# Kernel optimization log

Hardware: AMD Instinct MI355X
Metric: run time of the kernel (lower is better)

The kernel has to match this reference:

```python
import jax, jax.numpy as jnp
import numpy as np

NUM_HEADS = 8
DIM = 256
NUM_Q = 1


def setup_inputs() -> dict:
    key = jax.random.key(0)
    ks = jax.random.split(key, 10)
    B, H, W, C = 4, 56, 56, DIM
    mask_h = mask_w = 7
    WinNum = mask_h * mask_w
    x = jax.random.normal(ks[0], (B, H, W, C), dtype=jnp.float32)
    clstoken = jax.random.normal(ks[1], (B, NUM_Q, C), dtype=jnp.float32)
    mask = jax.random.bernoulli(ks[2], 0.3, (B, WinNum, WinNum))
    # ensure each window attends to itself (avoid fully-masked rows)
    eye = jnp.eye(WinNum, dtype=bool)[None]
    mask = jnp.logical_or(mask, eye)
    Wqkv = jax.random.normal(ks[3], (C, 3 * C), dtype=jnp.float32) * (C ** -0.5)
    bqkv = jnp.zeros((3 * C,), dtype=jnp.float32)
    Wo = jax.random.normal(ks[4], (C, C), dtype=jnp.float32) * (C ** -0.5)
    bo = jnp.zeros((C,), dtype=jnp.float32)
    lepe_k = jax.random.normal(ks[5], (3, 3, 1, C), dtype=jnp.float32) * 0.1  # depthwise HWIO
    lepe_b = jnp.zeros((C,), dtype=jnp.float32)
    return {"x": x, "clstoken": clstoken, "mask": mask, "mask_h": mask_h,
            "mask_w": mask_w, "Wqkv": Wqkv, "bqkv": bqkv, "Wo": Wo, "bo": bo,
            "lepe_k": lepe_k, "lepe_b": lepe_b}


def _forward(x, clstoken, mask, mask_h, mask_w, Wqkv, bqkv, Wo, bo, lepe_k, lepe_b):
    B, H, W, C = x.shape
    num_q = clstoken.shape[1]
    Nh = NUM_HEADS
    Hd = C // Nh
    Win_h, Win_w = H // mask_h, W // mask_w
    WinPix = Win_h * Win_w
    WinNum = mask_h * mask_w
    L_win = H * W
    scale = C ** -0.5

    qkv = x @ Wqkv + bqkv                       # [B,H,W,3C]
    q, k, v = jnp.split(qkv, 3, axis=-1)
    qkv_cls = clstoken @ Wqkv + bqkv            # [B,Q,3C]
    q_cls, k_cls, v_cls = jnp.split(qkv_cls, 3, axis=-1)

    # depthwise lepe conv on v (NHWC)
    lepe = jax.lax.conv_general_dilated(
        v, lepe_k, window_strides=(1, 1), padding='SAME',
        dimension_numbers=('NHWC', 'HWIO', 'NHWC'), feature_group_count=C) + lepe_b

    def to_win(t):  # b (j h)(i w)(Nh Hd) -> b Nh (j i h w) Hd
        t = t.reshape(B, mask_h, Win_h, mask_w, Win_w, Nh, Hd)
        t = t.transpose(0, 5, 1, 3, 2, 4, 6)
        return t.reshape(B, Nh, L_win, Hd)

    def cls_heads(t):  # b q (Nh Hd) -> b Nh q Hd
        return t.reshape(B, num_q, Nh, Hd).transpose(0, 2, 1, 3)

    q_all = jnp.concatenate([to_win(q), cls_heads(q_cls)], axis=2)
    k_all = jnp.concatenate([to_win(k), cls_heads(k_cls)], axis=2)
    v_all = jnp.concatenate([to_win(v), cls_heads(v_cls)], axis=2)

    # token-level block mask; cls block (id WinNum) is globally visible
    blk = jnp.concatenate([jnp.arange(L_win) // WinPix,
                           jnp.full((num_q,), WinNum)])
    mask_ext = jnp.pad(mask, ((0, 0), (0, 1), (0, 1)), constant_values=True)
    tok_mask = mask_ext[:, blk[:, None], blk[None, :]]  # [B,L,L]

    scores = jnp.einsum('bnqd,bnkd->bnqk', q_all, k_all) * scale
    neg = jnp.finfo(scores.dtype).min
    scores = jnp.where(tok_mask[:, None], scores, neg)
    attn = jax.nn.softmax(scores, axis=-1)
    out = jnp.einsum('bnqk,bnkd->bnqd', attn, v_all)   # [B,Nh,L,Hd]

    cls_out = out[:, :, -num_q:, :]
    x_out = out[:, :, :-num_q, :]
    # b Nh (j i h w) Hd -> b (j h)(i w)(Nh Hd)
    x_out = x_out.reshape(B, Nh, mask_h, mask_w, Win_h, Win_w, Hd)
    x_out = x_out.transpose(0, 2, 4, 3, 5, 1, 6).reshape(B, H, W, C)
    cls_out = cls_out.transpose(0, 2, 1, 3).reshape(B, num_q, C)

    x_out = (x_out + lepe) @ Wo + bo
    cls_out = cls_out @ Wo + bo
    return x_out, cls_out


def reference(x, clstoken, mask, mask_h, mask_w, Wqkv, bqkv, Wo, bo, lepe_k, lepe_b):
    return _forward(x, clstoken, mask, mask_h, mask_w, Wqkv, bqkv, Wo, bo, lepe_k, lepe_b)
```

## Files before the change

kernel.cpp:

```cpp
#include <hip/hip_runtime.h>
#include <math.h>

#define B_      4
#define NH      8
#define HD      32
#define WINNUM  49
#define LWIN    3136
#define NTOK    3137
#define NPIX    12544
#define MROWS   12548
#define SCALE_L2E 0.09016844005556021f
#define SM_BIAS   4.0f

typedef _Float16 half_t;
using half8 = __attribute__((ext_vector_type(8))) half_t;
using half4 = __attribute__((ext_vector_type(4))) half_t;
using f32x4 = __attribute__((ext_vector_type(4))) float;

__device__ __forceinline__ unsigned pack2(float a, float b) {
    auto h = __builtin_amdgcn_cvt_pkrtz(a, b);
    return __builtin_bit_cast(unsigned, h);
}

__global__ __launch_bounds__(256)
void prep(const float* __restrict__ x, const float* __restrict__ cls,
          const float* __restrict__ Wqkv, const float* __restrict__ Wo,
          half_t* __restrict__ xh, half_t* __restrict__ Wqkvt, half_t* __restrict__ Wot)
{
    const int idx = blockIdx.x * 256 + threadIdx.x;
    const int stride = gridDim.x * 256;
    for (int i = idx; i < MROWS * 256; i += stride) {
        int row = i >> 8, c = i & 255;
        float v = (row < NPIX) ? x[i] : cls[(row - NPIX) * 256 + c];
        xh[i] = (half_t)v;
    }
    for (int i = idx; i < 768 * 256; i += stride) {
        int n = i >> 8, k = i & 255;
        Wqkvt[i] = (half_t)Wqkv[k * 768 + n];
    }
    for (int i = idx; i < 256 * 256; i += stride) {
        int n = i >> 8, k = i & 255;
        Wot[i] = (half_t)Wo[k * 256 + n];
    }
}

__global__ __launch_bounds__(256)
void qkv_gemm(const half_t* __restrict__ xh, const half_t* __restrict__ Bt,
              const float* __restrict__ bqkv,
              half_t* __restrict__ qh, half_t* __restrict__ kh,
              half_t* __restrict__ khcls, half_t* __restrict__ vh,
              half_t* __restrict__ vplain)
{
    __shared__ __align__(16) short As[2][128 * 40];
    __shared__ __align__(16) short Bs[2][128 * 40];
    const int m0 = blockIdx.y * 128, n0 = blockIdx.x * 128;
    const int tid = threadIdx.x;
    const int lane = tid & 63, wv = tid >> 6;
    const int wm = wv >> 1, wn = wv & 1;
    const int qi = lane & 15, g = lane >> 4;
    f32x4 acc[4][4] = {};

    int4 ra[2], rb[2];
    auto issue = [&](int k0) {
#pragma unroll
        for (int i = 0; i < 2; ++i) {
            int ch = tid + 256 * i;
            int row = ch >> 2, kc = (ch & 3) * 8;
            int m = m0 + row;
            ra[i] = (m < MROWS) ? *(const int4*)(xh + (size_t)m * 256 + k0 + kc)
                                : make_int4(0, 0, 0, 0);
            rb[i] = *(const int4*)(Bt + (size_t)(n0 + row) * 256 + k0 + kc);
        }
    };
    auto commit = [&](int bu) {
#pragma unroll
        for (int i = 0; i < 2; ++i) {
            int ch = tid + 256 * i;
            int row = ch >> 2, kc = (ch & 3) * 8;
            *(int4*)&As[bu][row * 40 + kc] = ra[i];
            *(int4*)&Bs[bu][row * 40 + kc] = rb[i];
        }
    };

    issue(0); commit(0);
    __syncthreads();
    int buf = 0;
    for (int s = 0; s < 8; ++s) {
        if (s < 7) issue((s + 1) * 32);
        half8 af[4], bf[4];
#pragma unroll
        for (int f = 0; f < 4; ++f) {
            af[f] = *(const half8*)&As[buf][(wm * 64 + f * 16 + qi) * 40 + g * 8];
            bf[f] = *(const half8*)&Bs[buf][(wn * 64 + f * 16 + qi) * 40 + g * 8];
        }
#pragma unroll
        for (int fm = 0; fm < 4; ++fm)
#pragma unroll
            for (int fn = 0; fn < 4; ++fn)
                acc[fm][fn] = __builtin_amdgcn_mfma_f32_16x16x32_f16(af[fm], bf[fn], acc[fm][fn], 0, 0, 0);
        if (s < 7) commit(buf ^ 1);
        __syncthreads();
        buf ^= 1;
    }

    const int part = n0 >> 8;
    int nhv[4], dv[4];
    float bq[4];
#pragma unroll
    for (int fn = 0; fn < 4; ++fn) {
        int n = n0 + wn * 64 + fn * 16 + qi;
        bq[fn] = bqkv[n];
        int c = n & 255;
        nhv[fn] = c >> 5; dv[fn] = c & 31;
    }
#pragma unroll
    for (int fm = 0; fm < 4; ++fm) {
#pragma unroll
        for (int r = 0; r < 4; ++r) {
            int m = m0 + wm * 64 + fm * 16 + g * 4 + r;
            if (m >= MROWS) continue;
            int b, tok;
            if (m < NPIX) {
                b = m / LWIN;
                int p = m - b * LWIN;
                int hh = p / 56, ww = p - hh * 56;
                tok = ((hh >> 3) * 7 + (ww >> 3)) * 64 + ((hh & 7) << 3) + (ww & 7);
            } else { b = m - NPIX; tok = LWIN; }
#pragma unroll
            for (int fn = 0; fn < 4; ++fn) {
                float val = acc[fm][fn][r] + bq[fn];
                size_t bh = (size_t)(b * NH + nhv[fn]);
                int d = dv[fn];
                if (part == 0) {
                    qh[(bh * NTOK + tok) * 32 + d] = (half_t)(val * SCALE_L2E);
                } else if (part == 1) {
                    if (tok < LWIN) kh[(bh * WINNUM + (tok >> 6)) * 2560 + (tok & 63) * 40 + d] = (half_t)val;
                    else            khcls[bh * 32 + d] = (half_t)val;
                } else {
                    vplain[(bh * NTOK + tok) * 32 + d] = (half_t)val;
                    if (tok < LWIN) vh[(bh * WINNUM + (tok >> 6)) * 2560 + d * 80 + (tok & 63)] = (half_t)val;
                }
            }
        }
    }
}

__global__ __launch_bounds__(256)
void win_attn(const half_t* __restrict__ qh, const half_t* __restrict__ kh,
              const half_t* __restrict__ khcls, const half_t* __restrict__ vh,
              const half_t* __restrict__ vplain, const int* __restrict__ mask,
              half_t* __restrict__ tg, float* __restrict__ clspart)
{
    const int id = blockIdx.x;
    const int tid = threadIdx.x;
    __shared__ __align__(16) int4 KV[2][640];
    __shared__ __align__(16) short Plds[4][16 * 72];
    const int lane = tid & 63, wv = tid >> 6;

    if (id >= 1568) {
        const int cid = id - 1568;
        const int bh = cid >> 3;
        const int chunk = cid & 7;
        const int wstart = chunk * 6;
        const int nw = (chunk < 7) ? 6 : 7;
        const int nkeys = nw * 64;

        float q[32];
        {
            const half_t* qp = qh + ((size_t)bh * NTOK + LWIN) * 32;
#pragma unroll
            for (int d = 0; d < 32; ++d) q[d] = (float)qp[d];
        }
        float l = 0.f, o[32];
#pragma unroll
        for (int d = 0; d < 32; ++d) o[d] = 0.f;

        const half_t* kwb = kh + (size_t)bh * (WINNUM * 2560) + wstart * 2560;
        const half_t* vb  = vplain + ((size_t)bh * NTOK + wstart * 64) * 32;

        for (int kk = tid; kk < nkeys; kk += 256) {
            const half_t* kp = kwb + (kk >> 6) * 2560 + (kk & 63) * 40;
            float s = 0.f;
#pragma unroll
            for (int c8 = 0; c8 < 4; ++c8) {
                half8 kv = *(const half8*)(kp + c8 * 8);
#pragma unroll
                for (int j = 0; j < 8; ++j) s += q[c8 * 8 + j] * (float)kv[j];
            }
            float pp = exp2f(s - SM_BIAS);
            l += pp;
            const half_t* vp = vb + (size_t)kk * 32;
#pragma unroll
            for (int c8 = 0; c8 < 4; ++c8) {
                half8 vv = *(const half8*)(vp + c8 * 8);
#pragma unroll
                for (int j = 0; j < 8; ++j) o[c8 * 8 + j] += pp * (float)vv[j];
            }
        }
        if (chunk == 7 && tid == 0) {
            const half_t* kp = khcls + bh * 32;
            float s = 0.f;
#pragma unroll
            for (int d = 0; d < 32; ++d) s += q[d] * (float)kp[d];
            float pp = exp2f(s - SM_BIAS);
            l += pp;
            const half_t* vp = vplain + ((size_t)bh * NTOK + LWIN) * 32;
#pragma unroll
            for (int d = 0; d < 32; ++d) o[d] += pp * (float)vp[d];
        }
#pragma unroll
        for (int off = 1; off < 64; off <<= 1) {
            l += __shfl_xor(l, off);
#pragma unroll
            for (int d = 0; d < 32; ++d) o[d] += __shfl_xor(o[d], off);
        }
        float* red = (float*)&KV[0][0];
        if (lane == 0) {
#pragma unroll
            for (int d = 0; d < 32; ++d) red[wv * 33 + d] = o[d];
            red[wv * 33 + 32] = l;
        }
        __syncthreads();
        if (tid < 33) {
            float s = red[tid] + red[33 + tid] + red[66 + tid] + red[99 + tid];
            clspart[(bh * 8 + chunk) * 33 + tid] = s;
        }
        return;
    }

    const int sw = (id & 7) * 196 + (id >> 3);
    const int wi = sw % 49;
    const int bh = sw / 49;
    const int b = bh >> 3, nh = bh & 7;

    const int g = lane >> 4, qi = lane & 15;
    const int qrow = wi * 64 + wv * 16 + qi;

    half8 aq = *(const half8*)(qh + ((size_t)bh * NTOK + qrow) * 32 + g * 8);
    float qf[8];
#pragma unroll
    for (int j = 0; j < 8; ++j) qf[j] = (float)aq[j];
    float kcls[8], vcls[2][4];
#pragma unroll
    for (int j = 0; j < 8; ++j) kcls[j] = (float)khcls[bh * 32 + g * 8 + j];
    {
        const half_t* vcb = vplain + ((size_t)bh * NTOK + LWIN) * 32;
#pragma unroll
        for (int h2 = 0; h2 < 2; ++h2)
#pragma unroll
            for (int r = 0; r < 4; ++r) vcls[h2][r] = (float)vcb[h2 * 16 + g * 4 + r];
    }

    float lacc = 0.f;
    f32x4 acc[2] = {{0.f,0.f,0.f,0.f},{0.f,0.f,0.f,0.f}};

    const int* mrow = mask + (b * WINNUM + wi) * WINNUM;
    int mv = (lane < WINNUM) ? mrow[lane] : 0;
    unsigned long long rem = __ballot(mv != 0);

    const int4* kwin = (const int4*)(kh + (size_t)bh * (WINNUM * 2560));
    const int4* vwin = (const int4*)(vh + (size_t)bh * (WINNUM * 2560));

    int4 r0, r1, r2;
    auto issue = [&](int wj) {
        const int4* kg4 = kwin + wj * 320;
        const int4* vg4 = vwin + wj * 320;
        r0 = kg4[tid];
        r1 = (tid < 64) ? kg4[tid + 256] : vg4[tid - 64];
        if (tid < 128) r2 = vg4[tid + 192];
    };
    auto commit = [&](int bu) {
        KV[bu][tid] = r0;
        KV[bu][tid + 256] = r1;
        if (tid < 128) KV[bu][tid + 512] = r2;
    };

    int buf = 0;
    if (rem) { issue(__builtin_ctzll(rem)); commit(0); }
    __syncthreads();

    while (rem) {
        rem &= rem - 1;
        if (rem) issue(__builtin_ctzll(rem));

        const short* Kb = (const short*)&KV[buf][0];
        const short* Vb = (const short*)&KV[buf][320];

        f32x4 st[4];
        __builtin_amdgcn_s_setprio(1);
#pragma unroll
        for (int t4 = 0; t4 < 4; ++t4) {
            half8 ak = *(const half8*)&Kb[(t4 * 16 + qi) * 40 + g * 8];
            st[t4] = __builtin_amdgcn_mfma_f32_16x16x32_f16(ak, aq, (f32x4){0.f,0.f,0.f,0.f}, 0, 0, 0);
        }
        __builtin_amdgcn_s_setprio(0);
        float p[4][4];
#pragma unroll
        for (int t4 = 0; t4 < 4; ++t4)
#pragma unroll
            for (int r = 0; r < 4; ++r) {
                p[t4][r] = exp2f(st[t4][r] - SM_BIAS);
                lacc += p[t4][r];
            }
        {
            short* pw = &Plds[wv][qi * 72];
#pragma unroll
            for (int t4 = 0; t4 < 4; ++t4)
#pragma unroll
                for (int r2 = 0; r2 < 2; ++r2)
                    *(unsigned*)&pw[t4 * 16 + g * 4 + r2 * 2] = pack2(p[t4][2 * r2], p[t4][2 * r2 + 1]);
        }
        __builtin_amdgcn_s_setprio(1);
#pragma unroll
        for (int s2 = 0; s2 < 2; ++s2) {
            half8 bp = *(const half8*)&Plds[wv][qi * 72 + s2 * 32 + g * 8];
#pragma unroll
            for (int h2 = 0; h2 < 2; ++h2) {
                half8 av = *(const half8*)&Vb[(h2 * 16 + qi) * 80 + s2 * 32 + g * 8];
                acc[h2] = __builtin_amdgcn_mfma_f32_16x16x32_f16(av, bp, acc[h2], 0, 0, 0);
            }
        }
        __builtin_amdgcn_s_setprio(0);

        if (rem) commit(buf ^ 1);
        __syncthreads();
        buf ^= 1;
    }

    float pc;
    {
        float sc = 0.f;
#pragma unroll
        for (int j = 0; j < 8; ++j) sc += qf[j] * kcls[j];
        sc += __shfl_xor(sc, 16);
        sc += __shfl_xor(sc, 32);
        pc = exp2f(sc - SM_BIAS);
    }
    lacc += __shfl_xor(lacc, 16);
    lacc += __shfl_xor(lacc, 32);
    float l = lacc + pc;
#pragma unroll
    for (int h2 = 0; h2 < 2; ++h2)
#pragma unroll
        for (int r = 0; r < 4; ++r) acc[h2][r] += pc * vcls[h2][r];

    {
        float inv = 1.f / l;
        int kk = wv * 16 + qi;
        int hh = (wi / 7) * 8 + (kk >> 3);
        int ww = (wi % 7) * 8 + (kk & 7);
        size_t pix = (size_t)b * LWIN + hh * 56 + ww;
        half_t* tp = tg + pix * 256 + nh * 32;
#pragma unroll
        for (int h2 = 0; h2 < 2; ++h2) {
            half4 hv;
#pragma unroll
            for (int r = 0; r < 4; ++r) hv[r] = (half_t)(acc[h2][r] * inv);
            *(half4*)(tp + h2 * 16 + g * 4) = hv;
        }
    }
}

__global__ __launch_bounds__(256)
void lepe_add(const half_t* __restrict__ vplain, const float* __restrict__ lk,
              const float* __restrict__ lb, const float* __restrict__ clspart,
              half_t* __restrict__ tg)
{
    if (blockIdx.x == 1568) {
        const int c = threadIdx.x;
        const int nh = c >> 5, d = c & 31;
#pragma unroll
        for (int b = 0; b < 4; ++b) {
            int bh = b * NH + nh;
            float os = 0.f, ls = 0.f;
#pragma unroll
            for (int ch = 0; ch < 8; ++ch) {
                os += clspart[(bh * 8 + ch) * 33 + d];
                ls += clspart[(bh * 8 + ch) * 33 + 32];
            }
            tg[(size_t)(NPIX + b) * 256 + c] = (half_t)(os / ls);
        }
        return;
    }
    const int gidx = blockIdx.x * 256 + threadIdx.x;
    const int pix = gidx >> 5, cg = gidx & 31;
    const int c0 = cg * 8;
    const int b = pix / LWIN, p = pix - b * LWIN;
    const int hh = p / 56, ww = p - hh * 56;
    const int nh = c0 >> 5, d0 = c0 & 31;
    const half_t* vb = vplain + (size_t)(b * NH + nh) * NTOK * 32 + d0;

    float s[8];
#pragma unroll
    for (int j = 0; j < 8; ++j) s[j] = lb[c0 + j];
#pragma unroll
    for (int dh = -1; dh <= 1; ++dh) {
        int hn = hh + dh;
        if (hn < 0 || hn >= 56) continue;
#pragma unroll
        for (int dw = -1; dw <= 1; ++dw) {
            int wn = ww + dw;
            if (wn < 0 || wn >= 56) continue;
            int tok = ((hn >> 3) * 7 + (wn >> 3)) * 64 + ((hn & 7) << 3) + (wn & 7);
            half8 vv = *(const half8*)(vb + (size_t)tok * 32);
            const float* kk = lk + ((dh + 1) * 3 + (dw + 1)) * 256 + c0;
#pragma unroll
            for (int j = 0; j < 8; ++j) s[j] += (float)vv[j] * kk[j];
        }
    }
    half_t* tp = tg + (size_t)pix * 256 + c0;
    half8 cur = *(const half8*)tp;
    half8 outv;
#pragma unroll
    for (int j = 0; j < 8; ++j) outv[j] = (half_t)((float)cur[j] + s[j]);
    *(half8*)tp = outv;
}

__global__ __launch_bounds__(256)
void out_gemm(const half_t* __restrict__ th, const half_t* __restrict__ Bt,
              const float* __restrict__ bo, float* __restrict__ out)
{
    __shared__ __align__(16) short As[2][128 * 40];
    __shared__ __align__(16) short Bs[2][128 * 40];
    const int m0 = blockIdx.y * 128, n0 = blockIdx.x * 128;
    const int tid = threadIdx.x;
    const int lane = tid & 63, wv = tid >> 6;
    const int wm = wv >> 1, wn = wv & 1;
    const int qi = lane & 15, g = lane >> 4;
    f32x4 acc[4][4] = {};

    int4 ra[2], rb[2];
    auto issue = [&](int k0) {
#pragma unroll
        for (int i = 0; i < 2; ++i) {
            int ch = tid + 256 * i;
            int row = ch >> 2, kc = (ch & 3) * 8;
            int m = m0 + row;
            ra[i] = (m < MROWS) ? *(const int4*)(th + (size_t)m * 256 + k0 + kc)
                                : make_int4(0, 0, 0, 0);
            rb[i] = *(const int4*)(Bt + (size_t)(n0 + row) * 256 + k0 + kc);
        }
    };
    auto commit = [&](int bu) {
#pragma unroll
        for (int i = 0; i < 2; ++i) {
            int ch = tid + 256 * i;
            int row = ch >> 2, kc = (ch & 3) * 8;
            *(int4*)&As[bu][row * 40 + kc] = ra[i];
            *(int4*)&Bs[bu][row * 40 + kc] = rb[i];
        }
    };

    issue(0); commit(0);
    __syncthreads();
    int buf = 0;
    for (int s = 0; s < 8; ++s) {
        if (s < 7) issue((s + 1) * 32);
        half8 af[4], bf[4];
#pragma unroll
        for (int f = 0; f < 4; ++f) {
            af[f] = *(const half8*)&As[buf][(wm * 64 + f * 16 + qi) * 40 + g * 8];
            bf[f] = *(const half8*)&Bs[buf][(wn * 64 + f * 16 + qi) * 40 + g * 8];
        }
#pragma unroll
        for (int fm = 0; fm < 4; ++fm)
#pragma unroll
            for (int fn = 0; fn < 4; ++fn)
                acc[fm][fn] = __builtin_amdgcn_mfma_f32_16x16x32_f16(af[fm], bf[fn], acc[fm][fn], 0, 0, 0);
        if (s < 7) commit(buf ^ 1);
        __syncthreads();
        buf ^= 1;
    }

    float bov[4];
    int nn[4];
#pragma unroll
    for (int fn = 0; fn < 4; ++fn) {
        nn[fn] = n0 + wn * 64 + fn * 16 + qi;
        bov[fn] = bo[nn[fn]];
    }
#pragma unroll
    for (int fm = 0; fm < 4; ++fm)
#pragma unroll
        for (int r = 0; r < 4; ++r) {
            int m = m0 + wm * 64 + fm * 16 + g * 4 + r;
            if (m >= MROWS) continue;
#pragma unroll
            for (int fn = 0; fn < 4; ++fn)
                out[(size_t)m * 256 + nn[fn]] = acc[fm][fn][r] + bov[fn];
        }
}

extern "C" void kernel_launch(void* const* d_in, const int* in_sizes, int n_in,
                              void* d_out, int out_size, void* d_ws, size_t ws_size,
                              hipStream_t stream)
{
    const float* x    = (const float*)d_in[0];
    const float* cls  = (const float*)d_in[1];
    const int*   mask = (const int*)d_in[2];
    const float* Wqkv = (const float*)d_in[5];
    const float* bqkv = (const float*)d_in[6];
    const float* Wo   = (const float*)d_in[7];
    const float* bo   = (const float*)d_in[8];
    const float* lk   = (const float*)d_in[9];
    const float* lb   = (const float*)d_in[10];
    float* out = (float*)d_out;

    char* w = (char*)d_ws;
    half_t* xh     = (half_t*)w;  w += 6424576;
    half_t* qh     = (half_t*)w;  w += 6424576;
    half_t* kh     = (half_t*)w;  w += 8028160;
    half_t* khcls  = (half_t*)w;  w += 2048;
    half_t* vh     = (half_t*)w;  w += 8028160;
    half_t* vplain = (half_t*)w;  w += 6424576;
    half_t* Wqkvt  = (half_t*)w;  w += 393216;
    half_t* Wot    = (half_t*)w;  w += 131072;
    half_t* th     = (half_t*)w;  w += 6424576;
    float*  clspart= (float*)w;   w += 33792;

    prep<<<1600, 256, 0, stream>>>(x, cls, Wqkv, Wo, xh, Wqkvt, Wot);
    qkv_gemm<<<dim3(6, 99), 256, 0, stream>>>(xh, Wqkvt, bqkv, qh, kh, khcls, vh, vplain);
    win_attn<<<1824, 256, 0, stream>>>(qh, kh, khcls, vh, vplain, mask, th, clspart);
    lepe_add<<<1569, 256, 0, stream>>>(vplain, lk, lb, clspart, th);
    out_gemm<<<dim3(2, 99), 256, 0, stream>>>(th, Wot, bo, out);
}
```

Before: 125.3 us.

## Split window attention key dimension across two wave groups with 512-thread blocks

```diff
diff --git a/kernel.cpp b/kernel.cpp
--- a/kernel.cpp
+++ b/kernel.cpp
@@ -145,7 +145,7 @@
     }
 }
 
-__global__ __launch_bounds__(256)
+__global__ __launch_bounds__(512)
 void win_attn(const half_t* __restrict__ qh, const half_t* __restrict__ kh,
               const half_t* __restrict__ khcls, const half_t* __restrict__ vh,
               const half_t* __restrict__ vplain, const int* __restrict__ mask,
@@ -178,8 +178,8 @@
         const half_t* kwb = kh + (size_t)bh * (WINNUM * 2560) + wstart * 2560;
         const half_t* vb  = vplain + ((size_t)bh * NTOK + wstart * 64) * 32;
 
-        for (int kk = tid; kk < nkeys; kk += 256) {
-            const half_t* kp = kwb + (kk >> 6) * 2560 + (kk & 63) * 40;
+        if (tid < nkeys) {
+            const half_t* kp = kwb + (tid >> 6) * 2560 + (tid & 63) * 40;
             float s = 0.f;
 #pragma unroll
             for (int c8 = 0; c8 < 4; ++c8) {
@@ -189,12 +189,12 @@
             }
             float pp = exp2f(s - SM_BIAS);
             l += pp;
-            const half_t* vp = vb + (size_t)kk * 32;
+            const half_t* vp = vb + (size_t)tid * 32;
 #pragma unroll
             for (int c8 = 0; c8 < 4; ++c8) {
-                half8 vv = *(const half8*)(vp + c8 * 8);
-#pragma unroll
-                for (int j = 0; j < 8; ++j) o[c8 * 8 + j] += pp * (float)vv[j];
+                half8 vvv = *(const half8*)(vp + c8 * 8);
+#pragma unroll
+                for (int j = 0; j < 8; ++j) o[c8 * 8 + j] += pp * (float)vvv[j];
             }
         }
         if (chunk == 7 && tid == 0) {
@@ -222,7 +222,9 @@
         }
         __syncthreads();
         if (tid < 33) {
-            float s = red[tid] + red[33 + tid] + red[66 + tid] + red[99 + tid];
+            float s = 0.f;
+#pragma unroll
+            for (int wq = 0; wq < 8; ++wq) s += red[wq * 33 + tid];
             clspart[(bh * 8 + chunk) * 33 + tid] = s;
         }
         return;
@@ -233,23 +235,11 @@
     const int bh = sw / 49;
     const int b = bh >> 3, nh = bh & 7;
 
+    const int wq = wv & 3, wk = wv >> 2;
     const int g = lane >> 4, qi = lane & 15;
-    const int qrow = wi * 64 + wv * 16 + qi;
+    const int qrow = wi * 64 + wq * 16 + qi;
 
     half8 aq = *(const half8*)(qh + ((size_t)bh * NTOK + qrow) * 32 + g * 8);
-    float qf[8];
-#pragma unroll
-    for (int j = 0; j < 8; ++j) qf[j] = (float)aq[j];
-    float kcls[8], vcls[2][4];
-#pragma unroll
-    for (int j = 0; j < 8; ++j) kcls[j] = (float)khcls[bh * 32 + g * 8 + j];
-    {
-        const half_t* vcb = vplain + ((size_t)bh * NTOK + LWIN) * 32;
-#pragma unroll
-        for (int h2 = 0; h2 < 2; ++h2)
-#pragma unroll
-            for (int r = 0; r < 4; ++r) vcls[h2][r] = (float)vcb[h2 * 16 + g * 4 + r];
-    }
 
     float lacc = 0.f;
     f32x4 acc[2] = {{0.f,0.f,0.f,0.f},{0.f,0.f,0.f,0.f}};
@@ -261,18 +251,14 @@
     const int4* kwin = (const int4*)(kh + (size_t)bh * (WINNUM * 2560));
     const int4* vwin = (const int4*)(vh + (size_t)bh * (WINNUM * 2560));
 
-    int4 r0, r1, r2;
+    int4 r0, r1;
     auto issue = [&](int wj) {
-        const int4* kg4 = kwin + wj * 320;
-        const int4* vg4 = vwin + wj * 320;
-        r0 = kg4[tid];
-        r1 = (tid < 64) ? kg4[tid + 256] : vg4[tid - 64];
-        if (tid < 128) r2 = vg4[tid + 192];
+        r0 = (tid < 320) ? kwin[wj * 320 + tid] : vwin[wj * 320 + tid - 320];
+        if (tid < 128) r1 = vwin[wj * 320 + 192 + tid];
     };
     auto commit = [&](int bu) {
         KV[bu][tid] = r0;
-        KV[bu][tid + 256] = r1;
-        if (tid < 128) KV[bu][tid + 512] = r2;
+        if (tid < 128) KV[bu][512 + tid] = r1;
     };
 
     int buf = 0;
@@ -286,37 +272,36 @@
         const short* Kb = (const short*)&KV[buf][0];
         const short* Vb = (const short*)&KV[buf][320];
 
-        f32x4 st[4];
+        f32x4 st[2];
         __builtin_amdgcn_s_setprio(1);
 #pragma unroll
-        for (int t4 = 0; t4 < 4; ++t4) {
-            half8 ak = *(const half8*)&Kb[(t4 * 16 + qi) * 40 + g * 8];
-            st[t4] = __builtin_amdgcn_mfma_f32_16x16x32_f16(ak, aq, (f32x4){0.f,0.f,0.f,0.f}, 0, 0, 0);
+        for (int t = 0; t < 2; ++t) {
+            half8 ak = *(const half8*)&Kb[((2 * wk + t) * 16 + qi) * 40 + g * 8];
+            st[t] = __builtin_amdgcn_mfma_f32_16x16x32_f16(ak, aq, (f32x4){0.f,0.f,0.f,0.f}, 0, 0, 0);
         }
         __builtin_amdgcn_s_setprio(0);
-        float p[4][4];
-#pragma unroll
-        for (int t4 = 0; t4 < 4; ++t4)
+        float p[2][4];
+#pragma unroll
+        for (int t = 0; t < 2; ++t)
 #pragma unroll
             for (int r = 0; r < 4; ++r) {
-                p[t4][r] = exp2f(st[t4][r] - SM_BIAS);
-                lacc += p[t4][r];
+                p[t][r] = exp2f(st[t][r] - SM_BIAS);
+                lacc += p[t][r];
             }
         {
-            short* pw = &Plds[wv][qi * 72];
-#pragma unroll
-            for (int t4 = 0; t4 < 4; ++t4)
+            short* pw = &Plds[wq][qi * 72];
+#pragma unroll
+            for (int t = 0; t < 2; ++t)
 #pragma unroll
                 for (int r2 = 0; r2 < 2; ++r2)
-                    *(unsigned*)&pw[t4 * 16 + g * 4 + r2 * 2] = pack2(p[t4][2 * r2], p[t4][2 * r2 + 1]);
+                    *(unsigned*)&pw[(2 * wk + t) * 16 + g * 4 + r2 * 2] = pack2(p[t][2 * r2], p[t][2 * r2 + 1]);
         }
         __builtin_amdgcn_s_setprio(1);
-#pragma unroll
-        for (int s2 = 0; s2 < 2; ++s2) {
-            half8 bp = *(const half8*)&Plds[wv][qi * 72 + s2 * 32 + g * 8];
+        {
+            half8 bp = *(const half8*)&Plds[wq][qi * 72 + wk * 32 + g * 8];
 #pragma unroll
             for (int h2 = 0; h2 < 2; ++h2) {
-                half8 av = *(const half8*)&Vb[(h2 * 16 + qi) * 80 + s2 * 32 + g * 8];
+                half8 av = *(const half8*)&Vb[(h2 * 16 + qi) * 80 + wk * 32 + g * 8];
                 acc[h2] = __builtin_amdgcn_mfma_f32_16x16x32_f16(av, bp, acc[h2], 0, 0, 0);
             }
         }
@@ -327,26 +312,52 @@
         buf ^= 1;
     }
 
-    float pc;
-    {
+    lacc += __shfl_xor(lacc, 16);
+    lacc += __shfl_xor(lacc, 32);
+
+    __syncthreads();
+    float* comb = (float*)Plds;
+    if (wk == 1) {
+#pragma unroll
+        for (int h2 = 0; h2 < 2; ++h2)
+#pragma unroll
+            for (int r = 0; r < 4; ++r)
+                comb[wq * 544 + (h2 * 16 + g * 4 + r) * 16 + qi] = acc[h2][r];
+        if (g == 0) comb[wq * 544 + 512 + qi] = lacc;
+    }
+    __syncthreads();
+    if (wk == 0) {
+#pragma unroll
+        for (int h2 = 0; h2 < 2; ++h2)
+#pragma unroll
+            for (int r = 0; r < 4; ++r)
+                acc[h2][r] += comb[wq * 544 + (h2 * 16 + g * 4 + r) * 16 + qi];
+        float l = lacc + comb[wq * 544 + 512 + qi];
+
+        float kcls[8], vcls[2][4];
+#pragma unroll
+        for (int j = 0; j < 8; ++j) kcls[j] = (float)khcls[bh * 32 + g * 8 + j];
+        {
+            const half_t* vcb = vplain + ((size_t)bh * NTOK + LWIN) * 32;
+#pragma unroll
+            for (int h2 = 0; h2 < 2; ++h2)
+#pragma unroll
+                for (int r = 0; r < 4; ++r) vcls[h2][r] = (float)vcb[h2 * 16 + g * 4 + r];
+        }
         float sc = 0.f;
 #pragma unroll
-        for (int j = 0; j < 8; ++j) sc += qf[j] * kcls[j];
+        for (int j = 0; j < 8; ++j) sc += (float)aq[j] * kcls[j];
         sc += __shfl_xor(sc, 16);
         sc += __shfl_xor(sc, 32);
-        pc = exp2f(sc - SM_BIAS);
-    }
-    lacc += __shfl_xor(lacc, 16);
-    lacc += __shfl_xor(lacc, 32);
-    float l = lacc + pc;
-#pragma unroll
-    for (int h2 = 0; h2 < 2; ++h2)
-#pragma unroll
-        for (int r = 0; r < 4; ++r) acc[h2][r] += pc * vcls[h2][r];
-
-    {
+        float pc = exp2f(sc - SM_BIAS);
+        l += pc;
+#pragma unroll
+        for (int h2 = 0; h2 < 2; ++h2)
+#pragma unroll
+            for (int r = 0; r < 4; ++r) acc[h2][r] += pc * vcls[h2][r];
+
         float inv = 1.f / l;
-        int kk = wv * 16 + qi;
+        int kk = wq * 16 + qi;
         int hh = (wi / 7) * 8 + (kk >> 3);
         int ww = (wi % 7) * 8 + (kk & 7);
         size_t pix = (size_t)b * LWIN + hh * 56 + ww;
@@ -402,10 +413,10 @@
             int wn = ww + dw;
             if (wn < 0 || wn >= 56) continue;
             int tok = ((hn >> 3) * 7 + (wn >> 3)) * 64 + ((hn & 7) << 3) + (wn & 7);
-            half8 vv = *(const half8*)(vb + (size_t)tok * 32);
+            half8 vvv = *(const half8*)(vb + (size_t)tok * 32);
             const float* kk = lk + ((dh + 1) * 3 + (dw + 1)) * 256 + c0;
 #pragma unroll
-            for (int j = 0; j < 8; ++j) s[j] += (float)vv[j] * kk[j];
+            for (int j = 0; j < 8; ++j) s[j] += (float)vvv[j] * kk[j];
         }
     }
     half_t* tp = tg + (size_t)pix * 256 + c0;
@@ -520,7 +531,7 @@
 
     prep<<<1600, 256, 0, stream>>>(x, cls, Wqkv, Wo, xh, Wqkvt, Wot);
     qkv_gemm<<<dim3(6, 99), 256, 0, stream>>>(xh, Wqkvt, bqkv, qh, kh, khcls, vh, vplain);
-    win_attn<<<1824, 256, 0, stream>>>(qh, kh, khcls, vh, vplain, mask, th, clspart);
+    win_attn<<<1824, 512, 0, stream>>>(qh, kh, khcls, vh, vplain, mask, th, clspart);
     lepe_add<<<1569, 256, 0, stream>>>(vplain, lk, lb, clspart, th);
     out_gemm<<<dim3(2, 99), 256, 0, stream>>>(th, Wot, bo, out);
 }
```

New measurement: 130.6 us. 1.04x slower.

## Load K/V fragments directly from global into registers, drop LDS staging

Applied to the files above, without the earlier changes.

```diff
diff --git a/kernel.cpp b/kernel.cpp
--- a/kernel.cpp
+++ b/kernel.cpp
@@ -20,6 +20,9 @@
 __device__ __forceinline__ unsigned pack2(float a, float b) {
     auto h = __builtin_amdgcn_cvt_pkrtz(a, b);
     return __builtin_bit_cast(unsigned, h);
+}
+__device__ __forceinline__ half8 as_h8(int4 v) {
+    return __builtin_bit_cast(half8, v);
 }
 
 __global__ __launch_bounds__(256)
@@ -153,8 +156,8 @@
 {
     const int id = blockIdx.x;
     const int tid = threadIdx.x;
-    __shared__ __align__(16) int4 KV[2][640];
     __shared__ __align__(16) short Plds[4][16 * 72];
+    __shared__ float redc[4 * 33];
     const int lane = tid & 63, wv = tid >> 6;
 
     if (id >= 1568) {
@@ -192,9 +195,9 @@
             const half_t* vp = vb + (size_t)kk * 32;
 #pragma unroll
             for (int c8 = 0; c8 < 4; ++c8) {
-                half8 vv = *(const half8*)(vp + c8 * 8);
-#pragma unroll
-                for (int j = 0; j < 8; ++j) o[c8 * 8 + j] += pp * (float)vv[j];
+                half8 vvv = *(const half8*)(vp + c8 * 8);
+#pragma unroll
+                for (int j = 0; j < 8; ++j) o[c8 * 8 + j] += pp * (float)vvv[j];
             }
         }
         if (chunk == 7 && tid == 0) {
@@ -214,15 +217,14 @@
 #pragma unroll
             for (int d = 0; d < 32; ++d) o[d] += __shfl_xor(o[d], off);
         }
-        float* red = (float*)&KV[0][0];
         if (lane == 0) {
 #pragma unroll
-            for (int d = 0; d < 32; ++d) red[wv * 33 + d] = o[d];
-            red[wv * 33 + 32] = l;
+            for (int d = 0; d < 32; ++d) redc[wv * 33 + d] = o[d];
+            redc[wv * 33 + 32] = l;
         }
         __syncthreads();
         if (tid < 33) {
-            float s = red[tid] + red[33 + tid] + red[66 + tid] + red[99 + tid];
+            float s = redc[tid] + redc[33 + tid] + redc[66 + tid] + redc[99 + tid];
             clspart[(bh * 8 + chunk) * 33 + tid] = s;
         }
         return;
@@ -237,9 +239,67 @@
     const int qrow = wi * 64 + wv * 16 + qi;
 
     half8 aq = *(const half8*)(qh + ((size_t)bh * NTOK + qrow) * 32 + g * 8);
-    float qf[8];
-#pragma unroll
-    for (int j = 0; j < 8; ++j) qf[j] = (float)aq[j];
+
+    float lacc = 0.f;
+    f32x4 acc[2] = {{0.f,0.f,0.f,0.f},{0.f,0.f,0.f,0.f}};
+
+    const int* mrow = mask + (b * WINNUM + wi) * WINNUM;
+    int mv = (lane < WINNUM) ? mrow[lane] : 0;
+    unsigned long long rem = __ballot(mv != 0);
+
+    const half_t* kwin = kh + (size_t)bh * (WINNUM * 2560);
+    const half_t* vwin = vh + (size_t)bh * (WINNUM * 2560);
+    const int koff = qi * 40 + g * 8;
+    const int voff = qi * 80 + g * 8;
+
+    short* pw = &Plds[wv][qi * 72];
+    const short* prd = &Plds[wv][qi * 72 + g * 8];
+
+    while (rem) {
+        const int wj = __builtin_ctzll(rem);
+        rem &= rem - 1;
+        const half_t* kb = kwin + wj * 2560 + koff;
+        const half_t* vb = vwin + wj * 2560 + voff;
+        int4 kf0 = *(const int4*)(kb);
+        int4 kf1 = *(const int4*)(kb + 640);
+        int4 kf2 = *(const int4*)(kb + 1280);
+        int4 kf3 = *(const int4*)(kb + 1920);
+        int4 vf00 = *(const int4*)(vb);
+        int4 vf01 = *(const int4*)(vb + 32);
+        int4 vf10 = *(const int4*)(vb + 1280);
+        int4 vf11 = *(const int4*)(vb + 1312);
+
+        f32x4 st[4];
+        __builtin_amdgcn_s_setprio(1);
+        st[0] = __builtin_amdgcn_mfma_f32_16x16x32_f16(as_h8(kf0), aq, (f32x4){0.f,0.f,0.f,0.f}, 0, 0, 0);
+        st[1] = __builtin_amdgcn_mfma_f32_16x16x32_f16(as_h8(kf1), aq, (f32x4){0.f,0.f,0.f,0.f}, 0, 0, 0);
+        st[2] = __builtin_amdgcn_mfma_f32_16x16x32_f16(as_h8(kf2), aq, (f32x4){0.f,0.f,0.f,0.f}, 0, 0, 0);
+        st[3] = __builtin_amdgcn_mfma_f32_16x16x32_f16(as_h8(kf3), aq, (f32x4){0.f,0.f,0.f,0.f}, 0, 0, 0);
+        __builtin_amdgcn_s_setprio(0);
+
+#pragma unroll
+        for (int t = 0; t < 4; ++t) {
+            float p0 = exp2f(st[t][0] - SM_BIAS);
+            float p1 = exp2f(st[t][1] - SM_BIAS);
+            float p2 = exp2f(st[t][2] - SM_BIAS);
+            float p3 = exp2f(st[t][3] - SM_BIAS);
+            lacc += (p0 + p1) + (p2 + p3);
+            uint2 pk = make_uint2(pack2(p0, p1), pack2(p2, p3));
+            *(uint2*)&pw[t * 16 + 4 * g] = pk;
+        }
+        half8 bp0 = *(const half8*)(prd);
+        half8 bp1 = *(const half8*)(prd + 32);
+        __builtin_amdgcn_s_setprio(1);
+        acc[0] = __builtin_amdgcn_mfma_f32_16x16x32_f16(as_h8(vf00), bp0, acc[0], 0, 0, 0);
+        acc[1] = __builtin_amdgcn_mfma_f32_16x16x32_f16(as_h8(vf10), bp0, acc[1], 0, 0, 0);
+        acc[0] = __builtin_amdgcn_mfma_f32_16x16x32_f16(as_h8(vf01), bp1, acc[0], 0, 0, 0);
+        acc[1] = __builtin_amdgcn_mfma_f32_16x16x32_f16(as_h8(vf11), bp1, acc[1], 0, 0, 0);
+        __builtin_amdgcn_s_setprio(0);
+    }
+
+    lacc += __shfl_xor(lacc, 16);
+    lacc += __shfl_xor(lacc, 32);
+
     float kcls[8], vcls[2][4];
 #pragma unroll
     for (int j = 0; j < 8; ++j) kcls[j] = (float)khcls[bh * 32 + g * 8 + j];
@@ -250,94 +310,12 @@
 #pragma unroll
             for (int r = 0; r < 4; ++r) vcls[h2][r] = (float)vcb[h2 * 16 + g * 4 + r];
     }
-
-    float lacc = 0.f;
-    f32x4 acc[2] = {{0.f,0.f,0.f,0.f},{0.f,0.f,0.f,0.f}};
-
-    const int* mrow = mask + (b * WINNUM + wi) * WINNUM;
-    int mv = (lane < WINNUM) ? mrow[lane] : 0;
-    unsigned long long rem = __ballot(mv != 0);
-
-    const int4* kwin = (const int4*)(kh + (size_t)bh * (WINNUM * 2560));
-    const int4* vwin = (const int4*)(vh + (size_t)bh * (WINNUM * 2560));
-
-    int4 r0, r1, r2;
-    auto issue = [&](int wj) {
-        const int4* kg4 = kwin + wj * 320;
-        const int4* vg4 = vwin + wj * 320;
-        r0 = kg4[tid];
-        r1 = (tid < 64) ? kg4[tid + 256] : vg4[tid - 64];
-        if (tid < 128) r2 = vg4[tid + 192];
-    };
-    auto commit = [&](int bu) {
-        KV[bu][tid] = r0;
-        KV[bu][tid + 256] = r1;
-        if (tid < 128) KV[bu][tid + 512] = r2;
-    };
-
-    int buf = 0;
-    if (rem) { issue(__builtin_ctzll(rem)); commit(0); }
-    __syncthreads();
-
-    while (rem) {
-        rem &= rem - 1;
-        if (rem) issue(__builtin_ctzll(rem));
-
-        const short* Kb = (const short*)&KV[buf][0];
-        const short* Vb = (const short*)&KV[buf][320];
-
-        f32x4 st[4];
-        __builtin_amdgcn_s_setprio(1);
-#pragma unroll
-        for (int t4 = 0; t4 < 4; ++t4) {
-            half8 ak = *(const half8*)&Kb[(t4 * 16 + qi) * 40 + g * 8];
-            st[t4] = __builtin_amdgcn_mfma_f32_16x16x32_f16(ak, aq, (f32x4){0.f,0.f,0.f,0.f}, 0, 0, 0);
-        }
-        __builtin_amdgcn_s_setprio(0);
-        float p[4][4];
-#pragma unroll
-        for (int t4 = 0; t4 < 4; ++t4)
-#pragma unroll
-            for (int r = 0; r < 4; ++r) {
-                p[t4][r] = exp2f(st[t4][r] - SM_BIAS);
-                lacc += p[t4][r];
-            }
-        {
-            short* pw = &Plds[wv][qi * 72];
-#pragma unroll
-            for (int t4 = 0; t4 < 4; ++t4)
-#pragma unroll
-                for (int r2 = 0; r2 < 2; ++r2)
-                    *(unsigned*)&pw[t4 * 16 + g * 4 + r2 * 2] = pack2(p[t4][2 * r2], p[t4][2 * r2 + 1]);
-        }
-        __builtin_amdgcn_s_setprio(1);
-#pragma unroll
-        for (int s2 = 0; s2 < 2; ++s2) {
-            half8 bp = *(const half8*)&Plds[wv][qi * 72 + s2 * 32 + g * 8];
-#pragma unroll
-            for (int h2 = 0; h2 < 2; ++h2) {
-                half8 av = *(const half8*)&Vb[(h2 * 16 + qi) * 80 + s2 * 32 + g * 8];
-                acc[h2] = __builtin_amdgcn_mfma_f32_16x16x32_f16(av, bp, acc[h2], 0, 0, 0);
-            }
-        }
-        __builtin_amdgcn_s_setprio(0);
-
-        if (rem) commit(buf ^ 1);
-        __syncthreads();
-        buf ^= 1;
-    }
-
-    float pc;
-    {
-        float sc = 0.f;
-#pragma unroll
-        for (int j = 0; j < 8; ++j) sc += qf[j] * kcls[j];
-        sc += __shfl_xor(sc, 16);
-        sc += __shfl_xor(sc, 32);
-        pc = exp2f(sc - SM_BIAS);
-    }
-    lacc += __shfl_xor(lacc, 16);
-    lacc += __shfl_xor(lacc, 32);
+    float sc = 0.f;
+#pragma unroll
+    for (int j = 0; j < 8; ++j) sc += (float)aq[j] * kcls[j];
+    sc += __shfl_xor(sc, 16);
+    sc += __shfl_xor(sc, 32);
+    float pc = exp2f(sc - SM_BIAS);
     float l = lacc + pc;
 #pragma unroll
     for (int h2 = 0; h2 < 2; ++h2)
@@ -402,10 +380,10 @@
             int wn = ww + dw;
             if (wn < 0 || wn >= 56) continue;
             int tok = ((hn >> 3) * 7 + (wn >> 3)) * 64 + ((hn & 7) << 3) + (wn & 7);
-            half8 vv = *(const half8*)(vb + (size_t)tok * 32);
+            half8 vvv = *(const half8*)(vb + (size_t)tok * 32);
             const float* kk = lk + ((dh + 1) * 3 + (dw + 1)) * 256 + c0;
 #pragma unroll
-            for (int j = 0; j < 8; ++j) s[j] += (float)vv[j] * kk[j];
+            for (int j = 0; j < 8; ++j) s[j] += (float)vvv[j] * kk[j];
         }
     }
     half_t* tp = tg + (size_t)pix * 256 + c0;
```

Result: faster. 122.1 us (-2.5%).
